# Kernel optimization log

Hardware: AMD Instinct MI355X
Metric: run time of the kernel (lower is better)

## Reference

```python
import jax, jax.numpy as jnp
import numpy as np

N_NODES = 100000
N_EDGES = 3200000
IN_DIM, HID1, HID2 = 128, 32, 16


def setup_inputs() -> dict:
    key = jax.random.key(0)
    ks = jax.random.split(key, 4)
    x = jax.random.normal(ks[0], (N_NODES, IN_DIM), dtype=jnp.float32)
    # glorot-ish scaling for weights
    W1 = jax.random.normal(ks[1], (IN_DIM, HID1), dtype=jnp.float32) * (1.0 / np.sqrt(IN_DIM))
    b1 = jnp.zeros((HID1,), dtype=jnp.float32)
    W2 = jax.random.normal(ks[2], (HID1, HID2), dtype=jnp.float32) * (1.0 / np.sqrt(HID1))
    b2 = jnp.zeros((HID2,), dtype=jnp.float32)
    edge_index = jax.random.randint(ks[3], (2, N_EDGES), 0, N_NODES, dtype=jnp.int64)
    return {"x": x, "W1": W1, "b1": b1, "W2": W2, "b2": b2, "edge_index": edge_index}


def _gcn_norm(edge_index, n_nodes):
    # add self loops, then symmetric normalization D^-1/2 (A+I) D^-1/2
    loops = jnp.arange(n_nodes, dtype=edge_index.dtype)
    src = jnp.concatenate([edge_index[0], loops])  # [E+N]
    dst = jnp.concatenate([edge_index[1], loops])
    deg = jax.ops.segment_sum(jnp.ones_like(dst, dtype=jnp.float32), dst, num_segments=n_nodes)
    inv_sqrt = jnp.where(deg > 0, jax.lax.rsqrt(jnp.maximum(deg, 1.0)), 0.0)
    norm = inv_sqrt[src] * inv_sqrt[dst]  # [E+N]
    return src, dst, norm


def _gcn_conv(x, W, b, src, dst, norm, n_nodes):
    xw = x @ W                                   # [N, out] transform first (out < in)
    msg = xw[src] * norm[:, None]                # gather + scale  [E+N, out]
    agg = jax.ops.segment_sum(msg, dst, num_segments=n_nodes)  # scatter-add
    return agg + b


def reference(x, W1, b1, W2, b2, edge_index):
    n = x.shape[0]
    src, dst, norm = _gcn_norm(edge_index, n)  # cached=True: same norm both layers
    h = _gcn_conv(x, W1, b1, src, dst, norm, n)
    h = jax.nn.relu(h)
    out = _gcn_conv(h, W2, b2, src, dst, norm, n)
    return out
```

## Files before the change

kernel.cpp:

```cpp
#include <hip/hip_runtime.h>


#define IN_DIM 128
#define HID1 32
#define HID2 16

#define BSHIFT 8
#define MAXNB 1024
#define SLABCAP 9216
#define P2_TILE 4096
#define P2_PER_THREAD 16

__device__ __forceinline__ float4 f4add(float4 a, float4 b) {
    a.x += b.x; a.y += b.y; a.z += b.z; a.w += b.w; return a;
}

__device__ __forceinline__ void load_edge(const int* __restrict__ e32, int is64,
                                          long e, long E, int& s, int& d) {
    if (is64) { s = e32[2 * e];  d = e32[2 * E + 2 * e]; }
    else      { s = e32[e];      d = e32[E + e]; }
}

__global__ void init_cursors(const int* __restrict__ e32, int* __restrict__ flag,
                             int* __restrict__ bucketCursor, int NB) {
    int i = blockIdx.x * blockDim.x + threadIdx.x;
    if (i < NB) bucketCursor[i] = i * SLABCAP;
    if (blockIdx.x == 0 && threadIdx.x == 0) {
        int is64 = 1;
        for (int k = 0; k < 64; ++k)
            if (e32[2 * k + 1] != 0) { is64 = 0; break; }
        *flag = is64;
    }
}

__global__ __launch_bounds__(256) void partition_edges(const int* __restrict__ e32,
                                                       const int* __restrict__ flag,
                                                       int* __restrict__ bucketCursor,
                                                       unsigned int* __restrict__ part,
                                                       int E, int NB) {
    __shared__ int lbase[MAXNB];
    for (int i = threadIdx.x; i < NB; i += 256) lbase[i] = 0;
    __syncthreads();
    int is64 = *flag;
    long e0 = (long)blockIdx.x * P2_TILE;
    unsigned int v[P2_PER_THREAD];
    int bb[P2_PER_THREAD];
#pragma unroll
    for (int i = 0; i < P2_PER_THREAD; ++i) {
        long e = e0 + threadIdx.x + i * 256;
        if (e < E) {
            int s, d;
            load_edge(e32, is64, e, E, s, d);
            bb[i] = d >> BSHIFT;
            v[i] = (unsigned int)s | ((unsigned int)(d & ((1 << BSHIFT) - 1)) << 17);
            atomicAdd(&lbase[bb[i]], 1);
        } else {
            bb[i] = -1;
        }
    }
    __syncthreads();
    for (int i = threadIdx.x; i < NB; i += 256) {
        int c = lbase[i];
        lbase[i] = c ? atomicAdd(&bucketCursor[i], c) : 0;
    }
    __syncthreads();
#pragma unroll
    for (int i = 0; i < P2_PER_THREAD; ++i) {
        if (bb[i] >= 0) {
            int pos = atomicAdd(&lbase[bb[i]], 1);
            if (pos < (bb[i] + 1) * SLABCAP)
                part[pos] = v[i];
        }
    }
}

__global__ void scan_buckets(const int* __restrict__ bucketCursor,
                             int* __restrict__ bucketStart, int NB) {
    int lane = threadIdx.x;
    int c[16];
    int sum = 0;
#pragma unroll
    for (int k = 0; k < 16; ++k) {
        int idx = lane * 16 + k;
        int sz = 0;
        if (idx < NB) {
            sz = bucketCursor[idx] - idx * SLABCAP;
            if (sz > SLABCAP) sz = SLABCAP;
        }
        c[k] = sz;
        sum += sz;
    }
    int s = sum;
#pragma unroll
    for (int off = 1; off < 64; off <<= 1) {
        int t = __shfl_up(s, off, 64);
        if (lane >= off) s += t;
    }
    int run = s - sum;
#pragma unroll
    for (int k = 0; k < 16; ++k) {
        int idx = lane * 16 + k;
        if (idx < NB) bucketStart[idx] = run;
        run += c[k];
    }
}

__global__ __launch_bounds__(256) void build_rows(const unsigned int* __restrict__ part,
                                                  const int* __restrict__ bucketCursor,
                                                  const int* __restrict__ bucketStart,
                                                  int* __restrict__ rowStart,
                                                  int* __restrict__ cnt,
                                                  float* __restrict__ inv,
                                                  int* __restrict__ srcs, int N) {
    int b = blockIdx.x;
    int sbeg = b * SLABCAP;
    int size = bucketCursor[b] - sbeg;
    if (size > SLABCAP) size = SLABCAP;
    int send = sbeg + size;
    int gbase = bucketStart[b];
    __shared__ int lc[256];
    __shared__ int lofs[256];
    __shared__ int wsum[4];
    int tid = threadIdx.x;
    lc[tid] = 0;
    __syncthreads();
    for (int i = sbeg + tid; i < send; i += 256)
        atomicAdd(&lc[part[i] >> 17], 1);
    __syncthreads();
    int c = lc[tid];
    int s = c;
#pragma unroll
    for (int off = 1; off < 64; off <<= 1) {
        int t = __shfl_up(s, off, 64);
        if ((tid & 63) >= off) s += t;
    }
    if ((tid & 63) == 63) wsum[tid >> 6] = s;
    __syncthreads();
    int wb = 0;
    for (int w = 0; w < (tid >> 6); ++w) wb += wsum[w];
    int gstart = gbase + wb + s - c;
    int n = (b << BSHIFT) + tid;
    if (n < N) {
        rowStart[n] = gstart;
        cnt[n] = c;
        inv[n] = rsqrtf((float)(c + 1));
    }
    lofs[tid] = gstart;
    __syncthreads();
    for (int i = sbeg + tid; i < send; i += 256) {
        unsigned int v = part[i];
        int pos = atomicAdd(&lofs[v >> 17], 1);
        srcs[pos] = (int)(v & 0x1FFFF);
    }
}

__global__ __launch_bounds__(256) void gemm1(const float* __restrict__ x,
                                             const float* __restrict__ W1,
                                             const float* __restrict__ inv,
                                             float* __restrict__ xw, int N) {
    __shared__ float4 sW4[IN_DIM * 8];
    for (int i = threadIdx.x; i < IN_DIM * 8; i += 256)
        sW4[i] = ((const float4*)W1)[i];
    __syncthreads();

    int rq = threadIdx.x >> 3;
    int cq = threadIdx.x & 7;
    int r0 = blockIdx.x * 128 + rq * 4;
    const float4* x4 = (const float4*)x;
    const float4 z4 = make_float4(0.f, 0.f, 0.f, 0.f);

    float4 acc[4];
#pragma unroll
    for (int i = 0; i < 4; ++i) acc[i] = z4;

    for (int k4 = 0; k4 < IN_DIM / 4; ++k4) {
        float4 xa[4];
#pragma unroll
        for (int i = 0; i < 4; ++i) {
            int r = r0 + i;
            xa[i] = (r < N) ? x4[(size_t)r * 32 + k4] : z4;
        }
#pragma unroll
        for (int kk = 0; kk < 4; ++kk) {
            float4 w = sW4[(k4 * 4 + kk) * 8 + cq];
#pragma unroll
            for (int i = 0; i < 4; ++i) {
                float xs = (kk == 0) ? xa[i].x : (kk == 1) ? xa[i].y
                         : (kk == 2) ? xa[i].z : xa[i].w;
                acc[i].x += xs * w.x;
                acc[i].y += xs * w.y;
                acc[i].z += xs * w.z;
                acc[i].w += xs * w.w;
            }
        }
    }

#pragma unroll
    for (int i = 0; i < 4; ++i) {
        int r = r0 + i;
        if (r <= N) {
            float s = (r < N) ? inv[r] : 0.f;
            float4 o;
            o.x = acc[i].x * s; o.y = acc[i].y * s;
            o.z = acc[i].z * s; o.w = acc[i].w * s;
            ((float4*)xw)[(size_t)r * 8 + cq] = o;
        }
    }
}

__global__ __launch_bounds__(256) void agg1_k(const int* __restrict__ rowStart,
                                              const int* __restrict__ cnt,
                                              const int* __restrict__ srcs,
                                              const float* __restrict__ inv,
                                              const float* __restrict__ xw,
                                              const float* __restrict__ b1,
                                              const float* __restrict__ W2,
                                              float* __restrict__ hw, int N) {
    __shared__ float sW2[HID1 * HID2];
    __shared__ float sAgg[4][HID1];
    for (int i = threadIdx.x; i < HID1 * HID2; i += 256) sW2[i] = W2[i];

    int w    = threadIdx.x >> 6;
    int lane = threadIdx.x & 63;
    int node = blockIdx.x * 4 + w;
    int nr   = (node < N) ? node : 0;
    int start = rowStart[nr];
    int len   = (node < N) ? cnt[nr] : 0;
    float invn = (node < N) ? inv[nr] : 0.f;
    int eg = lane >> 3;
    int r  = lane & 7;
    const float4* xw4 = (const float4*)xw;

    float4 acc = make_float4(0.f, 0.f, 0.f, 0.f);
    if (eg == 0) acc = xw4[(size_t)nr * 8 + r];

    int sv = (lane < len) ? srcs[start + lane] : N;
#pragma unroll
    for (int g = 0; g < 8; ++g) {
        int jb = g * 8;
        if (jb < len) {
            int s = __shfl(sv, jb + eg, 64);
            acc = f4add(acc, xw4[(size_t)s * 8 + r]);
        }
    }
    for (int j = 64 + eg; j < len; j += 8)
        acc = f4add(acc, xw4[(size_t)srcs[start + j] * 8 + r]);

#pragma unroll
    for (int off = 32; off >= 8; off >>= 1) {
        acc.x += __shfl_down(acc.x, off, 64);
        acc.y += __shfl_down(acc.y, off, 64);
        acc.z += __shfl_down(acc.z, off, 64);
        acc.w += __shfl_down(acc.w, off, 64);
    }
    if (lane < 8) {
        float4 bb = ((const float4*)b1)[lane];
        float4 o;
        o.x = fmaxf(bb.x + invn * acc.x, 0.f);
        o.y = fmaxf(bb.y + invn * acc.y, 0.f);
        o.z = fmaxf(bb.z + invn * acc.z, 0.f);
        o.w = fmaxf(bb.w + invn * acc.w, 0.f);
        ((float4*)&sAgg[w][0])[lane] = o;
    }
    __syncthreads();

    if (lane < HID2 && node <= N) {
        float y = 0.f;
#pragma unroll
        for (int cc = 0; cc < HID1; ++cc)
            y += sAgg[w][cc] * sW2[cc * HID2 + lane];
        hw[(size_t)node * HID2 + lane] = y * invn;
    }
}

__global__ __launch_bounds__(256) void agg2_k(const int* __restrict__ rowStart,
                                              const int* __restrict__ cnt,
                                              const int* __restrict__ srcs,
                                              const float* __restrict__ inv,
                                              const float* __restrict__ hw,
                                              const float* __restrict__ b2,
                                              float* __restrict__ out, int N) {
    int wave = (blockIdx.x * blockDim.x + threadIdx.x) >> 6;
    int lane = threadIdx.x & 63;
    if (wave >= N) return;
    int n = wave;
    int eg = lane >> 2;
    int q  = lane & 3;
    int start = rowStart[n];
    int len   = cnt[n];
    float invn = inv[n];
    const float4* hw4 = (const float4*)hw;

    float4 acc = make_float4(0.f, 0.f, 0.f, 0.f);
    if (eg == 0) acc = hw4[(size_t)n * 4 + q];

    int sv = (lane < len) ? srcs[start + lane] : N;
#pragma unroll
    for (int g = 0; g < 4; ++g) {
        int jb = g * 16;
        if (jb < len) {
            int s = __shfl(sv, jb + eg, 64);
            acc = f4add(acc, hw4[(size_t)s * 4 + q]);
        }
    }
    for (int j = 64 + eg; j < len; j += 16)
        acc = f4add(acc, hw4[(size_t)srcs[start + j] * 4 + q]);

#pragma unroll
    for (int off = 32; off >= 4; off >>= 1) {
        acc.x += __shfl_down(acc.x, off, 64);
        acc.y += __shfl_down(acc.y, off, 64);
        acc.z += __shfl_down(acc.z, off, 64);
        acc.w += __shfl_down(acc.w, off, 64);
    }
    if (lane < 4) {
        float4 bb = ((const float4*)b2)[lane];
        float4 o;
        o.x = bb.x + invn * acc.x;
        o.y = bb.y + invn * acc.y;
        o.z = bb.z + invn * acc.z;
        o.w = bb.w + invn * acc.w;
        ((float4*)out)[(size_t)n * 4 + lane] = o;
    }
}

extern "C" void kernel_launch(void* const* d_in, const int* in_sizes, int n_in,
                              void* d_out, int out_size, void* d_ws, size_t ws_size,
                              hipStream_t stream) {
    const float* x  = (const float*)d_in[0];
    const float* W1 = (const float*)d_in[1];
    const float* b1 = (const float*)d_in[2];
    const float* W2 = (const float*)d_in[3];
    const float* b2 = (const float*)d_in[4];
    const int*  e32 = (const int*)d_in[5];
    float* out = (float*)d_out;

    const int N = in_sizes[0] / IN_DIM;
    const int E = in_sizes[5] / 2;
    const int Npad = ((N + 63) / 64) * 64;
    const int Epad = ((E + 63) / 64) * 64;
    const int NB   = (N + (1 << BSHIFT) - 1) >> BSHIFT;

    char* ws = (char*)d_ws;
    int*   flag         = (int*)ws;
    int*   bucketCursor = (int*)(ws + 256);
    int*   bucketStart  = bucketCursor + 1088;
    int*   cnt      = bucketStart + 1088;
    int*   rowStart = cnt + Npad;
    float* inv      = (float*)(rowStart + Npad);
    int*   srcs     = (int*)(inv + Npad);
    size_t slab = (size_t)NB * SLABCAP;
    size_t PXW  = slab > (size_t)Npad * HID1 ? slab : (size_t)Npad * HID1;
    unsigned int* part = (unsigned int*)(srcs + Epad);
    float* xw   = (float*)part;
    float* hw   = (float*)(srcs + Epad + PXW);

    init_cursors<<<(NB + 255) / 256, 256, 0, stream>>>(e32, flag, bucketCursor, NB);
    partition_edges<<<(E + P2_TILE - 1) / P2_TILE, 256, 0, stream>>>(
        e32, flag, bucketCursor, part, E, NB);
    scan_buckets<<<1, 64, 0, stream>>>(bucketCursor, bucketStart, NB);
    build_rows<<<NB, 256, 0, stream>>>(part, bucketCursor, bucketStart,
                                       rowStart, cnt, inv, srcs, N);

    gemm1<<<(N + 1 + 127) / 128, 256, 0, stream>>>(x, W1, inv, xw, N);
    agg1_k<<<(N + 1 + 3) / 4, 256, 0, stream>>>(rowStart, cnt, srcs, inv, xw, b1, W2, hw, N);
    agg2_k<<<(N + 3) / 4, 256, 0, stream>>>(rowStart, cnt, srcs, inv, hw, b2, out, N);
}
```

Measured before the change: 310.1 us.

## Replace CSR build with bucket-slab aggregation using shared-memory atomics

Drops the per-node CSR construction (bucket scan and build_rows) and aggregates directly over the destination-bucket slabs produced by partitioning, with 64-node buckets. A new lightweight kernel computes degrees from the slabs, and both aggregation kernels accumulate gathered features into shared-memory tiles with float atomics before applying bias, ReLU and the second matmul per node. Partitioning switches to a two-pass read with 1024-thread blocks instead of holding edges in registers. This removes a full scatter pass and the srcs array, at the cost of many LDS atomics and nondeterministic summation order.

```diff
diff --git a/kernel.cpp b/kernel.cpp
--- a/kernel.cpp
+++ b/kernel.cpp
@@ -5,15 +5,10 @@
 #define HID1 32
 #define HID2 16
 
-#define BSHIFT 8
-#define MAXNB 1024
-#define SLABCAP 9216
-#define P2_TILE 4096
-#define P2_PER_THREAD 16
-
-__device__ __forceinline__ float4 f4add(float4 a, float4 b) {
-    a.x += b.x; a.y += b.y; a.z += b.z; a.w += b.w; return a;
-}
+#define BSHIFT 6
+#define MAXNB 1600
+#define SLABCAP 2600
+#define P2T 16384
 
 __device__ __forceinline__ void load_edge(const int* __restrict__ e32, int is64,
                                           long e, long E, int& s, int& d) {
@@ -33,124 +28,53 @@
     }
 }
 
-__global__ __launch_bounds__(256) void partition_edges(const int* __restrict__ e32,
-                                                       const int* __restrict__ flag,
-                                                       int* __restrict__ bucketCursor,
-                                                       unsigned int* __restrict__ part,
-                                                       int E, int NB) {
+__global__ __launch_bounds__(1024) void partition_edges(const int* __restrict__ e32,
+                                                        const int* __restrict__ flag,
+                                                        int* __restrict__ bucketCursor,
+                                                        unsigned int* __restrict__ part,
+                                                        int E, int NB) {
     __shared__ int lbase[MAXNB];
-    for (int i = threadIdx.x; i < NB; i += 256) lbase[i] = 0;
+    for (int i = threadIdx.x; i < NB; i += 1024) lbase[i] = 0;
     __syncthreads();
     int is64 = *flag;
-    long e0 = (long)blockIdx.x * P2_TILE;
-    unsigned int v[P2_PER_THREAD];
-    int bb[P2_PER_THREAD];
-#pragma unroll
-    for (int i = 0; i < P2_PER_THREAD; ++i) {
-        long e = e0 + threadIdx.x + i * 256;
-        if (e < E) {
-            int s, d;
-            load_edge(e32, is64, e, E, s, d);
-            bb[i] = d >> BSHIFT;
-            v[i] = (unsigned int)s | ((unsigned int)(d & ((1 << BSHIFT) - 1)) << 17);
-            atomicAdd(&lbase[bb[i]], 1);
-        } else {
-            bb[i] = -1;
-        }
-    }
-    __syncthreads();
-    for (int i = threadIdx.x; i < NB; i += 256) {
-        int c = lbase[i];
-        lbase[i] = c ? atomicAdd(&bucketCursor[i], c) : 0;
-    }
-    __syncthreads();
-#pragma unroll
-    for (int i = 0; i < P2_PER_THREAD; ++i) {
-        if (bb[i] >= 0) {
-            int pos = atomicAdd(&lbase[bb[i]], 1);
-            if (pos < (bb[i] + 1) * SLABCAP)
-                part[pos] = v[i];
-        }
-    }
-}
-
-__global__ void scan_buckets(const int* __restrict__ bucketCursor,
-                             int* __restrict__ bucketStart, int NB) {
-    int lane = threadIdx.x;
-    int c[16];
-    int sum = 0;
-#pragma unroll
-    for (int k = 0; k < 16; ++k) {
-        int idx = lane * 16 + k;
-        int sz = 0;
-        if (idx < NB) {
-            sz = bucketCursor[idx] - idx * SLABCAP;
-            if (sz > SLABCAP) sz = SLABCAP;
-        }
-        c[k] = sz;
-        sum += sz;
-    }
-    int s = sum;
-#pragma unroll
-    for (int off = 1; off < 64; off <<= 1) {
-        int t = __shfl_up(s, off, 64);
-        if (lane >= off) s += t;
-    }
-    int run = s - sum;
-#pragma unroll
-    for (int k = 0; k < 16; ++k) {
-        int idx = lane * 16 + k;
-        if (idx < NB) bucketStart[idx] = run;
-        run += c[k];
-    }
-}
-
-__global__ __launch_bounds__(256) void build_rows(const unsigned int* __restrict__ part,
-                                                  const int* __restrict__ bucketCursor,
-                                                  const int* __restrict__ bucketStart,
-                                                  int* __restrict__ rowStart,
-                                                  int* __restrict__ cnt,
-                                                  float* __restrict__ inv,
-                                                  int* __restrict__ srcs, int N) {
+    long e0 = (long)blockIdx.x * P2T;
+    long eend = e0 + P2T; if (eend > E) eend = E;
+    for (long e = e0 + threadIdx.x; e < eend; e += 1024) {
+        int d = is64 ? e32[2 * E + 2 * e] : e32[E + e];
+        atomicAdd(&lbase[d >> BSHIFT], 1);
+    }
+    __syncthreads();
+    for (int b = threadIdx.x; b < NB; b += 1024) {
+        int c = lbase[b];
+        lbase[b] = c ? atomicAdd(&bucketCursor[b], c) : 0;
+    }
+    __syncthreads();
+    for (long e = e0 + threadIdx.x; e < eend; e += 1024) {
+        int s, d;
+        load_edge(e32, is64, e, E, s, d);
+        int b = d >> BSHIFT;
+        int pos = atomicAdd(&lbase[b], 1);
+        if (pos < (b + 1) * SLABCAP)
+            part[pos] = (unsigned int)s | ((unsigned int)(d & 63) << 17);
+    }
+}
+
+__global__ __launch_bounds__(256) void degrees(const unsigned int* __restrict__ part,
+                                               const int* __restrict__ bucketCursor,
+                                               float* __restrict__ inv, int N) {
     int b = blockIdx.x;
     int sbeg = b * SLABCAP;
     int size = bucketCursor[b] - sbeg;
     if (size > SLABCAP) size = SLABCAP;
-    int send = sbeg + size;
-    int gbase = bucketStart[b];
-    __shared__ int lc[256];
-    __shared__ int lofs[256];
-    __shared__ int wsum[4];
-    int tid = threadIdx.x;
-    lc[tid] = 0;
-    __syncthreads();
-    for (int i = sbeg + tid; i < send; i += 256)
-        atomicAdd(&lc[part[i] >> 17], 1);
-    __syncthreads();
-    int c = lc[tid];
-    int s = c;
-#pragma unroll
-    for (int off = 1; off < 64; off <<= 1) {
-        int t = __shfl_up(s, off, 64);
-        if ((tid & 63) >= off) s += t;
-    }
-    if ((tid & 63) == 63) wsum[tid >> 6] = s;
-    __syncthreads();
-    int wb = 0;
-    for (int w = 0; w < (tid >> 6); ++w) wb += wsum[w];
-    int gstart = gbase + wb + s - c;
-    int n = (b << BSHIFT) + tid;
-    if (n < N) {
-        rowStart[n] = gstart;
-        cnt[n] = c;
-        inv[n] = rsqrtf((float)(c + 1));
-    }
-    lofs[tid] = gstart;
-    __syncthreads();
-    for (int i = sbeg + tid; i < send; i += 256) {
-        unsigned int v = part[i];
-        int pos = atomicAdd(&lofs[v >> 17], 1);
-        srcs[pos] = (int)(v & 0x1FFFF);
+    __shared__ int lc[64];
+    if (threadIdx.x < 64) lc[threadIdx.x] = 0;
+    __syncthreads();
+    for (int i = threadIdx.x; i < size; i += 256)
+        atomicAdd(&lc[(part[sbeg + i] >> 17) & 63], 1);
+    __syncthreads();
+    if (threadIdx.x < 64) {
+        int n = (b << BSHIFT) + threadIdx.x;
+        if (n < N) inv[n] = rsqrtf((float)(lc[threadIdx.x] + 1));
     }
 }
 
@@ -208,119 +132,128 @@
     }
 }
 
-__global__ __launch_bounds__(256) void agg1_k(const int* __restrict__ rowStart,
-                                              const int* __restrict__ cnt,
-                                              const int* __restrict__ srcs,
+__global__ __launch_bounds__(256) void agg1_k(const unsigned int* __restrict__ part,
+                                              const int* __restrict__ bucketCursor,
                                               const float* __restrict__ inv,
                                               const float* __restrict__ xw,
                                               const float* __restrict__ b1,
                                               const float* __restrict__ W2,
                                               float* __restrict__ hw, int N) {
     __shared__ float sW2[HID1 * HID2];
-    __shared__ float sAgg[4][HID1];
-    for (int i = threadIdx.x; i < HID1 * HID2; i += 256) sW2[i] = W2[i];
-
-    int w    = threadIdx.x >> 6;
-    int lane = threadIdx.x & 63;
-    int node = blockIdx.x * 4 + w;
-    int nr   = (node < N) ? node : 0;
-    int start = rowStart[nr];
-    int len   = (node < N) ? cnt[nr] : 0;
-    float invn = (node < N) ? inv[nr] : 0.f;
-    int eg = lane >> 3;
-    int r  = lane & 7;
+    __shared__ float sB1[HID1];
+    __shared__ float aggF[64][33];
+    int tid = threadIdx.x;
+    for (int i = tid; i < HID1 * HID2; i += 256) sW2[i] = W2[i];
+    if (tid < HID1) sB1[tid] = b1[tid];
+    for (int i = tid; i < 64 * 33; i += 256) ((float*)aggF)[i] = 0.f;
+    __syncthreads();
+
+    int b = blockIdx.x;
+    int sbeg = b * SLABCAP;
+    int size = bucketCursor[b] - sbeg;
+    if (size > SLABCAP) size = SLABCAP;
+
+    int wid = tid >> 6, lane = tid & 63;
+    int eg = lane >> 3, r = lane & 7;
     const float4* xw4 = (const float4*)xw;
 
-    float4 acc = make_float4(0.f, 0.f, 0.f, 0.f);
-    if (eg == 0) acc = xw4[(size_t)nr * 8 + r];
-
-    int sv = (lane < len) ? srcs[start + lane] : N;
-#pragma unroll
-    for (int g = 0; g < 8; ++g) {
-        int jb = g * 8;
-        if (jb < len) {
-            int s = __shfl(sv, jb + eg, 64);
-            acc = f4add(acc, xw4[(size_t)s * 8 + r]);
-        }
-    }
-    for (int j = 64 + eg; j < len; j += 8)
-        acc = f4add(acc, xw4[(size_t)srcs[start + j] * 8 + r]);
-
-#pragma unroll
-    for (int off = 32; off >= 8; off >>= 1) {
-        acc.x += __shfl_down(acc.x, off, 64);
-        acc.y += __shfl_down(acc.y, off, 64);
-        acc.z += __shfl_down(acc.z, off, 64);
-        acc.w += __shfl_down(acc.w, off, 64);
-    }
-    if (lane < 8) {
-        float4 bb = ((const float4*)b1)[lane];
+    for (int base = wid * 64; base < size; base += 256) {
+        int idx = base + lane;
+        int pe = (idx < size) ? (int)part[sbeg + idx] : N;
+        int rem = size - base;
+#pragma unroll
+        for (int g = 0; g < 8; ++g) {
+            if (g * 8 < rem) {
+                int meta = __shfl(pe, g * 8 + eg, 64);
+                int s  = meta & 0x1FFFF;
+                int dl = (meta >> 17) & 63;
+                float4 v = xw4[(size_t)s * 8 + r];
+                atomicAdd(&aggF[dl][r * 4 + 0], v.x);
+                atomicAdd(&aggF[dl][r * 4 + 1], v.y);
+                atomicAdd(&aggF[dl][r * 4 + 2], v.z);
+                atomicAdd(&aggF[dl][r * 4 + 3], v.w);
+            }
+        }
+    }
+    __syncthreads();
+
+    int nl = tid >> 2, og = tid & 3;
+    int node = (b << BSHIFT) + nl;
+    if (node <= N) {
+        float invn = (node < N) ? inv[node] : 0.f;
+        float y0 = 0.f, y1 = 0.f, y2 = 0.f, y3 = 0.f;
+#pragma unroll
+        for (int cq = 0; cq < 8; ++cq) {
+            float4 xv = xw4[(size_t)node * 8 + cq];
+            float sv[4] = {xv.x, xv.y, xv.z, xv.w};
+#pragma unroll
+            for (int k = 0; k < 4; ++k) {
+                int c = cq * 4 + k;
+                float a = fmaxf(sB1[c] + invn * (aggF[nl][c] + sv[k]), 0.f);
+                y0 += a * sW2[c * HID2 + og * 4 + 0];
+                y1 += a * sW2[c * HID2 + og * 4 + 1];
+                y2 += a * sW2[c * HID2 + og * 4 + 2];
+                y3 += a * sW2[c * HID2 + og * 4 + 3];
+            }
+        }
         float4 o;
-        o.x = fmaxf(bb.x + invn * acc.x, 0.f);
-        o.y = fmaxf(bb.y + invn * acc.y, 0.f);
-        o.z = fmaxf(bb.z + invn * acc.z, 0.f);
-        o.w = fmaxf(bb.w + invn * acc.w, 0.f);
-        ((float4*)&sAgg[w][0])[lane] = o;
-    }
-    __syncthreads();
-
-    if (lane < HID2 && node <= N) {
-        float y = 0.f;
-#pragma unroll
-        for (int cc = 0; cc < HID1; ++cc)
-            y += sAgg[w][cc] * sW2[cc * HID2 + lane];
-        hw[(size_t)node * HID2 + lane] = y * invn;
-    }
-}
-
-__global__ __launch_bounds__(256) void agg2_k(const int* __restrict__ rowStart,
-                                              const int* __restrict__ cnt,
-                                              const int* __restrict__ srcs,
+        o.x = y0 * invn; o.y = y1 * invn; o.z = y2 * invn; o.w = y3 * invn;
+        ((float4*)hw)[(size_t)node * 4 + og] = o;
+    }
+}
+
+__global__ __launch_bounds__(256) void agg2_k(const unsigned int* __restrict__ part,
+                                              const int* __restrict__ bucketCursor,
                                               const float* __restrict__ inv,
                                               const float* __restrict__ hw,
                                               const float* __restrict__ b2,
                                               float* __restrict__ out, int N) {
-    int wave = (blockIdx.x * blockDim.x + threadIdx.x) >> 6;
-    int lane = threadIdx.x & 63;
-    if (wave >= N) return;
-    int n = wave;
-    int eg = lane >> 2;
-    int q  = lane & 3;
-    int start = rowStart[n];
-    int len   = cnt[n];
-    float invn = inv[n];
+    __shared__ float aggF[64][17];
+    int tid = threadIdx.x;
+    for (int i = tid; i < 64 * 17; i += 256) ((float*)aggF)[i] = 0.f;
+    __syncthreads();
+
+    int b = blockIdx.x;
+    int sbeg = b * SLABCAP;
+    int size = bucketCursor[b] - sbeg;
+    if (size > SLABCAP) size = SLABCAP;
+
+    int wid = tid >> 6, lane = tid & 63;
+    int eg = lane >> 2, q = lane & 3;
     const float4* hw4 = (const float4*)hw;
 
-    float4 acc = make_float4(0.f, 0.f, 0.f, 0.f);
-    if (eg == 0) acc = hw4[(size_t)n * 4 + q];
-
-    int sv = (lane < len) ? srcs[start + lane] : N;
-#pragma unroll
-    for (int g = 0; g < 4; ++g) {
-        int jb = g * 16;
-        if (jb < len) {
-            int s = __shfl(sv, jb + eg, 64);
-            acc = f4add(acc, hw4[(size_t)s * 4 + q]);
-        }
-    }
-    for (int j = 64 + eg; j < len; j += 16)
-        acc = f4add(acc, hw4[(size_t)srcs[start + j] * 4 + q]);
-
-#pragma unroll
-    for (int off = 32; off >= 4; off >>= 1) {
-        acc.x += __shfl_down(acc.x, off, 64);
-        acc.y += __shfl_down(acc.y, off, 64);
-        acc.z += __shfl_down(acc.z, off, 64);
-        acc.w += __shfl_down(acc.w, off, 64);
-    }
-    if (lane < 4) {
-        float4 bb = ((const float4*)b2)[lane];
+    for (int base = wid * 64; base < size; base += 256) {
+        int idx = base + lane;
+        int pe = (idx < size) ? (int)part[sbeg + idx] : N;
+        int rem = size - base;
+#pragma unroll
+        for (int g = 0; g < 4; ++g) {
+            if (g * 16 < rem) {
+                int meta = __shfl(pe, g * 16 + eg, 64);
+                int s  = meta & 0x1FFFF;
+                int dl = (meta >> 17) & 63;
+                float4 v = hw4[(size_t)s * 4 + q];
+                atomicAdd(&aggF[dl][q * 4 + 0], v.x);
+                atomicAdd(&aggF[dl][q * 4 + 1], v.y);
+                atomicAdd(&aggF[dl][q * 4 + 2], v.z);
+                atomicAdd(&aggF[dl][q * 4 + 3], v.w);
+            }
+        }
+    }
+    __syncthreads();
+
+    int nl = tid >> 2, og = tid & 3;
+    int node = (b << BSHIFT) + nl;
+    if (node < N) {
+        float invn = inv[node];
+        float4 hv = hw4[(size_t)node * 4 + og];
+        float4 bb = ((const float4*)b2)[og];
         float4 o;
-        o.x = bb.x + invn * acc.x;
-        o.y = bb.y + invn * acc.y;
-        o.z = bb.z + invn * acc.z;
-        o.w = bb.w + invn * acc.w;
-        ((float4*)out)[(size_t)n * 4 + lane] = o;
+        o.x = bb.x + invn * (aggF[nl][og * 4 + 0] + hv.x);
+        o.y = bb.y + invn * (aggF[nl][og * 4 + 1] + hv.y);
+        o.z = bb.z + invn * (aggF[nl][og * 4 + 2] + hv.z);
+        o.w = bb.w + invn * (aggF[nl][og * 4 + 3] + hv.w);
+        ((float4*)out)[(size_t)node * 4 + og] = o;
     }
 }
 
@@ -337,32 +270,23 @@
 
     const int N = in_sizes[0] / IN_DIM;
     const int E = in_sizes[5] / 2;
-    const int Npad = ((N + 63) / 64) * 64;
-    const int Epad = ((E + 63) / 64) * 64;
-    const int NB   = (N + (1 << BSHIFT) - 1) >> BSHIFT;
+    const int Npad = ((N + 127) / 128) * 128;
+    const int NB   = (N + 63) >> 6;
 
     char* ws = (char*)d_ws;
     int*   flag         = (int*)ws;
     int*   bucketCursor = (int*)(ws + 256);
-    int*   bucketStart  = bucketCursor + 1088;
-    int*   cnt      = bucketStart + 1088;
-    int*   rowStart = cnt + Npad;
-    float* inv      = (float*)(rowStart + Npad);
-    int*   srcs     = (int*)(inv + Npad);
-    size_t slab = (size_t)NB * SLABCAP;
-    size_t PXW  = slab > (size_t)Npad * HID1 ? slab : (size_t)Npad * HID1;
-    unsigned int* part = (unsigned int*)(srcs + Epad);
-    float* xw   = (float*)part;
-    float* hw   = (float*)(srcs + Epad + PXW);
+    float* inv          = (float*)(ws + 256 + 6656);
+    unsigned int* part  = (unsigned int*)(inv + Npad);
+    float* xw = (float*)(part + (size_t)NB * SLABCAP + 64);
+    float* hw = xw + (size_t)(Npad + 128) * HID1;
 
     init_cursors<<<(NB + 255) / 256, 256, 0, stream>>>(e32, flag, bucketCursor, NB);
-    partition_edges<<<(E + P2_TILE - 1) / P2_TILE, 256, 0, stream>>>(
+    partition_edges<<<(E + P2T - 1) / P2T, 1024, 0, stream>>>(
         e32, flag, bucketCursor, part, E, NB);
-    scan_buckets<<<1, 64, 0, stream>>>(bucketCursor, bucketStart, NB);
-    build_rows<<<NB, 256, 0, stream>>>(part, bucketCursor, bucketStart,
-                                       rowStart, cnt, inv, srcs, N);
+    degrees<<<NB, 256, 0, stream>>>(part, bucketCursor, inv, N);
 
     gemm1<<<(N + 1 + 127) / 128, 256, 0, stream>>>(x, W1, inv, xw, N);
-    agg1_k<<<(N + 1 + 3) / 4, 256, 0, stream>>>(rowStart, cnt, srcs, inv, xw, b1, W2, hw, N);
-    agg2_k<<<(N + 3) / 4, 256, 0, stream>>>(rowStart, cnt, srcs, inv, hw, b2, out, N);
-}
+    agg1_k<<<NB, 256, 0, stream>>>(part, bucketCursor, inv, xw, b1, W2, hw, N);
+    agg2_k<<<NB, 256, 0, stream>>>(part, bucketCursor, inv, hw, b2, out, N);
+}
```

Measured after the change: 1.084 ms. 3.49x slower.
